# Kernel optimization log

Hardware: AMD Instinct MI355X
Metric: run time of the kernel (lower is better)

## Reference

```python
import jax, jax.numpy as jnp
import numpy as np

B = 524288      # batch
V = 128         # VEC_SIZE
N_VECS = 3
R = 4           # REDUNDANCY
NC = 2          # n_choices


def setup_inputs() -> dict:
    key = jax.random.key(0)
    ks = jax.random.split(key, 9)
    inv = 1.0 / np.sqrt(N_VECS * V)
    a = jax.random.normal(ks[0], (B, V), jnp.float32)
    b = jax.random.normal(ks[1], (B, V), jnp.float32)
    c = jax.random.normal(ks[2], (B, V), jnp.float32)
    W_ff = jax.random.normal(ks[3], (R * NC, N_VECS * V), jnp.float32) * inv
    W_guard = jax.random.normal(ks[4], (R * NC, N_VECS * V), jnp.float32) * inv
    W1 = jax.random.normal(ks[5], (R, R ** NC), jnp.float32) * (1.0 / np.sqrt(R ** NC))
    b1 = jax.random.normal(ks[6], (R,), jnp.float32) * 0.1
    W2 = jax.random.normal(ks[7], (NC, R), jnp.float32) * (1.0 / np.sqrt(R))
    b2 = jax.random.normal(ks[8], (NC,), jnp.float32) * 0.1
    return {"a": a, "b": b, "c": c, "W_ff": W_ff, "W_guard": W_guard,
            "W1": W1, "b1": b1, "W2": W2, "b2": b2}


def reference(a, b, c, W_ff, W_guard, W1, b1, W2, b2):
    # op(3, vec_size): Choice(..., n_choices=2, redundancy=4, has_guard=True,
    # method='outer_projection') -> Fn((x0 - x1 + 1)/2) -> unsqueeze(-1)
    x = jnp.concatenate([a, b, c], axis=1)                 # [B, 3V] (torch.hstack)
    f = jax.nn.sigmoid(x @ W_ff.T)                          # [B, R*NC]
    g = jax.nn.sigmoid(x @ W_guard.T)                       # [B, R*NC]
    outs = f * g                                            # guard gating
    c0, c1 = outs[:, :R], outs[:, R:]                       # torch.chunk(outs, 2, dim=1)
    outer = jnp.einsum('za,zb->zab', c0, c1).reshape(-1, R * R)  # [B, R**2]
    h = jax.nn.relu(outer @ W1.T + b1)                      # [B, R]
    p = jax.nn.sigmoid(h @ W2.T + b2)                       # [B, 2]
    out = ((p[:, 0] - p[:, 1] + 1.0) * 0.5)[:, None]        # [B, 1]
    return out
```

## Files before the change

kernel.cpp:

```cpp
#include <hip/hip_runtime.h>
#include <math.h>

#define ROWS   256
#define V      128
#define NW     384
#define CHUNK  32
#define PAD    36

__device__ __forceinline__ float sigmoidf_(float x) {
    return 1.0f / (1.0f + expf(-x));
}

__global__ __launch_bounds__(256, 4)
void fused_ns_kernel(const float* __restrict__ ga,
                     const float* __restrict__ gb,
                     const float* __restrict__ gc,
                     const float* __restrict__ Wff,
                     const float* __restrict__ Wgd,
                     const float* __restrict__ W1,
                     const float* __restrict__ b1,
                     const float* __restrict__ W2,
                     const float* __restrict__ b2,
                     float* __restrict__ out)
{
    __shared__ float lds[ROWS * PAD];
    const int t = threadIdx.x;
    const long row0 = (long)blockIdx.x * ROWS;

    float accf[8] = {0,0,0,0,0,0,0,0};
    float accg[8] = {0,0,0,0,0,0,0,0};

    for (int s = 0; s < 3; ++s) {
        const float* arr = (s == 0) ? ga : ((s == 1) ? gb : gc);
        for (int cc = 0; cc < 4; ++cc) {
            const int colbase = cc * CHUNK;
            const int wcol    = s * V + colbase;

            __syncthreads();
            #pragma unroll
            for (int k = 0; k < 8; ++k) {
                const int f  = t + (k << 8);
                const int r  = f >> 3;
                const int c4 = f & 7;
                float4 v = ((const float4*)(arr + (row0 + r) * V + colbase))[c4];
                *((float4*)(&lds[r * PAD + (c4 << 2)])) = v;
            }
            __syncthreads();

            const float* xr = &lds[t * PAD];
            #pragma unroll
            for (int jj = 0; jj < CHUNK; jj += 4) {
                const float4 xv = *((const float4*)(xr + jj));
                #pragma unroll
                for (int k = 0; k < 8; ++k) {
                    const float* wf = Wff + k * NW + wcol + jj;
                    accf[k] = fmaf(xv.x, wf[0],
                               fmaf(xv.y, wf[1],
                                fmaf(xv.z, wf[2],
                                 fmaf(xv.w, wf[3], accf[k]))));
                    const float* wg = Wgd + k * NW + wcol + jj;
                    accg[k] = fmaf(xv.x, wg[0],
                               fmaf(xv.y, wg[1],
                                fmaf(xv.z, wg[2],
                                 fmaf(xv.w, wg[3], accg[k]))));
                }
            }
        }
    }

    float outs[8];
    #pragma unroll
    for (int k = 0; k < 8; ++k)
        outs[k] = sigmoidf_(accf[k]) * sigmoidf_(accg[k]);

    float h[4];
    #pragma unroll
    for (int r = 0; r < 4; ++r) {
        float acc = b1[r];
        #pragma unroll
        for (int aa = 0; aa < 4; ++aa)
            #pragma unroll
            for (int bb = 0; bb < 4; ++bb)
                acc = fmaf(outs[aa] * outs[4 + bb], W1[r * 16 + aa * 4 + bb], acc);
        h[r] = fmaxf(acc, 0.0f);
    }

    float p[2];
    #pragma unroll
    for (int cc2 = 0; cc2 < 2; ++cc2) {
        float acc = b2[cc2];
        #pragma unroll
        for (int r = 0; r < 4; ++r)
            acc = fmaf(h[r], W2[cc2 * 4 + r], acc);
        p[cc2] = sigmoidf_(acc);
    }

    out[row0 + t] = (p[0] - p[1] + 1.0f) * 0.5f;
}

extern "C" void kernel_launch(void* const* d_in, const int* in_sizes, int n_in,
                              void* d_out, int out_size, void* d_ws, size_t ws_size,
                              hipStream_t stream) {
    const float* a   = (const float*)d_in[0];
    const float* b   = (const float*)d_in[1];
    const float* c   = (const float*)d_in[2];
    const float* Wff = (const float*)d_in[3];
    const float* Wgd = (const float*)d_in[4];
    const float* W1  = (const float*)d_in[5];
    const float* b1  = (const float*)d_in[6];
    const float* W2  = (const float*)d_in[7];
    const float* b2  = (const float*)d_in[8];
    float* out = (float*)d_out;

    const int nrows = in_sizes[0] / V;
    const int grid  = nrows / ROWS;

    fused_ns_kernel<<<grid, ROWS, 0, stream>>>(a, b, c, Wff, Wgd, W1, b1, W2, b2, out);
}
```

Measured before the change: 857.7 us.

## Compute projections with split-bf16 MFMA instead of scalar FMA loops

Replaces the per-thread scalar FMA dot products with 16x16x32 bf16 MFMA instructions. Both the activations and the weights are split into high and low bf16 parts, and three MFMAs per chunk approximate fp32 accuracy. Weights are preloaded into registers once per wave, each wave processes 8 tiles of 16 rows, and the epilogue runs on 16 lanes after the accumulators are staged through LDS. The grid is hardcoded to 1024 blocks, which assumes the fixed batch size, and the kernel drops the LDS staging and block-wide syncs for direct global loads.

```diff
diff --git a/kernel.cpp b/kernel.cpp
--- a/kernel.cpp
+++ b/kernel.cpp
@@ -1,101 +1,108 @@
 #include <hip/hip_runtime.h>
 #include <math.h>
 
-#define ROWS   256
-#define V      128
-#define NW     384
-#define CHUNK  32
-#define PAD    36
+typedef __attribute__((ext_vector_type(8))) short bf16x8;
+typedef __attribute__((ext_vector_type(4))) float f32x4;
 
-__device__ __forceinline__ float sigmoidf_(float x) {
-    return 1.0f / (1.0f + expf(-x));
+#define V   128
+#define NW  384
+#define TILES_PER_WAVE  8
+#define WAVES_PER_BLOCK 4
+
+__device__ __forceinline__ float sigmoidf_(float x) { return 1.0f / (1.0f + expf(-x)); }
+
+__device__ __forceinline__ void split8(float4 u0, float4 u1, bf16x8& h, bf16x8& l) {
+    float uu[8] = {u0.x, u0.y, u0.z, u0.w, u1.x, u1.y, u1.z, u1.w};
+    #pragma unroll
+    for (int j = 0; j < 8; ++j) {
+        unsigned b  = __float_as_uint(uu[j]);
+        unsigned hb = b & 0xFFFF0000u;
+        float r = uu[j] - __uint_as_float(hb);
+        h[j] = (short)(b >> 16);
+        l[j] = (short)(__float_as_uint(r) >> 16);
+    }
 }
 
-__global__ __launch_bounds__(256, 4)
-void fused_ns_kernel(const float* __restrict__ ga,
-                     const float* __restrict__ gb,
-                     const float* __restrict__ gc,
-                     const float* __restrict__ Wff,
-                     const float* __restrict__ Wgd,
-                     const float* __restrict__ W1,
-                     const float* __restrict__ b1,
-                     const float* __restrict__ W2,
-                     const float* __restrict__ b2,
-                     float* __restrict__ out)
+__global__ __launch_bounds__(256)
+void fused_ns_mfma(const float* __restrict__ ga, const float* __restrict__ gb,
+                   const float* __restrict__ gc, const float* __restrict__ Wff,
+                   const float* __restrict__ Wgd, const float* __restrict__ W1,
+                   const float* __restrict__ b1,  const float* __restrict__ W2,
+                   const float* __restrict__ b2,  float* __restrict__ out)
 {
-    __shared__ float lds[ROWS * PAD];
-    const int t = threadIdx.x;
-    const long row0 = (long)blockIdx.x * ROWS;
+    __shared__ float lds[WAVES_PER_BLOCK][16][20];
+    const int t  = threadIdx.x & 63;
+    const int w  = threadIdx.x >> 6;
+    const int gw = blockIdx.x * WAVES_PER_BLOCK + w;
+    const int lr = t & 15;
+    const int kb = t >> 4;
 
-    float accf[8] = {0,0,0,0,0,0,0,0};
-    float accg[8] = {0,0,0,0,0,0,0,0};
+    const float* wrow = (lr < 8) ? (Wff + lr * NW) : (Wgd + (lr - 8) * NW);
+    bf16x8 wh[12], wl[12];
+    #pragma unroll
+    for (int kc = 0; kc < 12; ++kc) {
+        const float* p = wrow + kc * 32 + kb * 8;
+        float4 u0 = *(const float4*)(p);
+        float4 u1 = *(const float4*)(p + 4);
+        split8(u0, u1, wh[kc], wl[kc]);
+    }
 
-    for (int s = 0; s < 3; ++s) {
-        const float* arr = (s == 0) ? ga : ((s == 1) ? gb : gc);
-        for (int cc = 0; cc < 4; ++cc) {
-            const int colbase = cc * CHUNK;
-            const int wcol    = s * V + colbase;
+    float* buf = &lds[w][0][0];
 
-            __syncthreads();
+    #pragma unroll 1
+    for (int i = 0; i < TILES_PER_WAVE; ++i) {
+        const long row0 = ((long)gw * TILES_PER_WAVE + i) * 16;
+        const float* xa = ga + (row0 + lr) * V + kb * 8;
+        const float* xb = gb + (row0 + lr) * V + kb * 8;
+        const float* xc = gc + (row0 + lr) * V + kb * 8;
+
+        f32x4 acc = {0.f, 0.f, 0.f, 0.f};
+        #pragma unroll
+        for (int s = 0; s < 3; ++s) {
+            const float* xr = (s == 0) ? xa : ((s == 1) ? xb : xc);
             #pragma unroll
-            for (int k = 0; k < 8; ++k) {
-                const int f  = t + (k << 8);
-                const int r  = f >> 3;
-                const int c4 = f & 7;
-                float4 v = ((const float4*)(arr + (row0 + r) * V + colbase))[c4];
-                *((float4*)(&lds[r * PAD + (c4 << 2)])) = v;
-            }
-            __syncthreads();
-
-            const float* xr = &lds[t * PAD];
-            #pragma unroll
-            for (int jj = 0; jj < CHUNK; jj += 4) {
-                const float4 xv = *((const float4*)(xr + jj));
-                #pragma unroll
-                for (int k = 0; k < 8; ++k) {
-                    const float* wf = Wff + k * NW + wcol + jj;
-                    accf[k] = fmaf(xv.x, wf[0],
-                               fmaf(xv.y, wf[1],
-                                fmaf(xv.z, wf[2],
-                                 fmaf(xv.w, wf[3], accf[k]))));
-                    const float* wg = Wgd + k * NW + wcol + jj;
-                    accg[k] = fmaf(xv.x, wg[0],
-                               fmaf(xv.y, wg[1],
-                                fmaf(xv.z, wg[2],
-                                 fmaf(xv.w, wg[3], accg[k]))));
-                }
+            for (int cc = 0; cc < 4; ++cc) {
+                float4 u0 = *(const float4*)(xr + cc * 32);
+                float4 u1 = *(const float4*)(xr + cc * 32 + 4);
+                bf16x8 xh, xl;
+                split8(u0, u1, xh, xl);
+                const int kc = s * 4 + cc;
+                acc = __builtin_amdgcn_mfma_f32_16x16x32_bf16(xh, wh[kc], acc, 0, 0, 0);
+                acc = __builtin_amdgcn_mfma_f32_16x16x32_bf16(xh, wl[kc], acc, 0, 0, 0);
+                acc = __builtin_amdgcn_mfma_f32_16x16x32_bf16(xl, wh[kc], acc, 0, 0, 0);
             }
         }
-    }
 
-    float outs[8];
-    #pragma unroll
-    for (int k = 0; k < 8; ++k)
-        outs[k] = sigmoidf_(accf[k]) * sigmoidf_(accg[k]);
-
-    float h[4];
-    #pragma unroll
-    for (int r = 0; r < 4; ++r) {
-        float acc = b1[r];
-        #pragma unroll
-        for (int aa = 0; aa < 4; ++aa)
-            #pragma unroll
-            for (int bb = 0; bb < 4; ++bb)
-                acc = fmaf(outs[aa] * outs[4 + bb], W1[r * 16 + aa * 4 + bb], acc);
-        h[r] = fmaxf(acc, 0.0f);
-    }
-
-    float p[2];
-    #pragma unroll
-    for (int cc2 = 0; cc2 < 2; ++cc2) {
-        float acc = b2[cc2];
         #pragma unroll
         for (int r = 0; r < 4; ++r)
-            acc = fmaf(h[r], W2[cc2 * 4 + r], acc);
-        p[cc2] = sigmoidf_(acc);
+            buf[(kb * 4 + r) * 20 + lr] = acc[r];
+
+        if (t < 16) {
+            const float* rp = buf + t * 20;
+            float o8[8];
+            #pragma unroll
+            for (int j = 0; j < 8; ++j)
+                o8[j] = sigmoidf_(rp[j]) * sigmoidf_(rp[8 + j]);
+            float hh[4];
+            #pragma unroll
+            for (int r = 0; r < 4; ++r) {
+                float a1 = b1[r];
+                #pragma unroll
+                for (int aa = 0; aa < 4; ++aa)
+                    #pragma unroll
+                    for (int bb = 0; bb < 4; ++bb)
+                        a1 = fmaf(o8[aa] * o8[4 + bb], W1[r * 16 + aa * 4 + bb], a1);
+                hh[r] = fmaxf(a1, 0.f);
+            }
+            float p0 = b2[0], p1 = b2[1];
+            #pragma unroll
+            for (int r = 0; r < 4; ++r) {
+                p0 = fmaf(hh[r], W2[r], p0);
+                p1 = fmaf(hh[r], W2[4 + r], p1);
+            }
+            out[row0 + t] = (sigmoidf_(p0) - sigmoidf_(p1) + 1.f) * 0.5f;
+        }
     }
-
-    out[row0 + t] = (p[0] - p[1] + 1.0f) * 0.5f;
 }
 
 extern "C" void kernel_launch(void* const* d_in, const int* in_sizes, int n_in,
@@ -112,8 +119,7 @@
     const float* b2  = (const float*)d_in[8];
     float* out = (float*)d_out;
 
-    const int nrows = in_sizes[0] / V;
-    const int grid  = nrows / ROWS;
-
-    fused_ns_kernel<<<grid, ROWS, 0, stream>>>(a, b, c, Wff, Wgd, W1, b1, W2, b2, out);
+    const int grid = 1024;
+    fused_ns_mfma<<<grid, 64 * WAVES_PER_BLOCK, 0, stream>>>(
+        a, b, c, Wff, Wgd, W1, b1, W2, b2, out);
 }
```

Measured after the change: 716.3 us. 1.2x faster.
